# Performance work log

Measured on AMD Instinct MI355X. Metric: run time of the kernel, lower is better.

The kernel has to match this reference:

```python
import jax, jax.numpy as jnp
import numpy as np

EPS = 1e-8

def setup_inputs() -> dict:
    key = jax.random.key(0)
    ks = jax.random.split(key, 10)
    N, IN, Z, C, H = 8192, 512, 128, 64, 50
    x = jax.random.normal(ks[0], (N, IN), dtype=jnp.float32)
    c = jax.random.randint(ks[1], (N, 1), 0, C, dtype=jnp.int64)
    z = jax.random.normal(ks[2], (N, Z), dtype=jnp.float32)
    # f_x MLP params (Linear(IN,50) -> ReLU -> Linear(50,Z))
    W1 = jax.random.normal(ks[3], (IN, H), dtype=jnp.float32) / np.sqrt(IN)
    b1 = jax.random.normal(ks[4], (H,), dtype=jnp.float32) * 0.01
    W2 = jax.random.normal(ks[5], (H, Z), dtype=jnp.float32) / np.sqrt(H)
    b2 = jax.random.normal(ks[6], (Z,), dtype=jnp.float32) * 0.01
    # f_z Linear(Z,Z)
    Wz = jax.random.normal(ks[7], (Z, Z), dtype=jnp.float32) / np.sqrt(Z)
    bz = jax.random.normal(ks[8], (Z,), dtype=jnp.float32) * 0.01
    # per-category bilinear weights w_s [C,Z,Z] (torch.randn init)
    Ws = jax.random.normal(ks[9], (C, Z, Z), dtype=jnp.float32)
    return {"x": x, "c": c, "z": z, "W1": W1, "b1": b1, "W2": W2, "b2": b2, "Wz": Wz, "bz": bz, "Ws": Ws}

def reference(x, c, z, W1, b1, W2, b2, Wz, bz, Ws):
    cf = c.reshape(-1)                                    # [N]
    fx = jax.nn.relu(x @ W1 + b1) @ W2 + b2               # [N,Z]
    fz = z @ Wz + bz                                      # [N,Z]
    # per-sample bilinear: u[n] = fx[n] @ Ws[c[n]]
    u = jnp.einsum('nd,nde->ne', fx, Ws[cf])              # [N,Z]
    T = jax.nn.softplus(jnp.einsum('ne,ne->n', u, fz))    # [N]
    # neg_T[i] = mean over j with c[j]==c[i] of softplus(fx[i] @ Ws[c[i]] @ fz[j])
    S = jax.nn.softplus(u @ fz.T)                         # [N,N]
    mask = (cf[:, None] == cf[None, :]).astype(S.dtype)   # [N,N]
    neg_T = (S * mask).sum(axis=1) / mask.sum(axis=1)     # [N]
    return jnp.log(T + EPS) - jnp.log(neg_T + EPS)
```

## Files before the change

### kernel.cpp

```cpp
#include <hip/hip_runtime.h>
#include <math.h>

#define N_   8192
#define IN_  512
#define ZD   128
#define CC   64
#define HD   50
#define EPSF 1e-8f

typedef float vf4 __attribute__((ext_vector_type(4)));
typedef __attribute__((ext_vector_type(8))) short bfrag;

#define MFMA16(a, b, c) __builtin_amdgcn_mfma_f32_16x16x32_bf16((a), (b), (c), 0, 0, 0)

__device__ __forceinline__ float softplus_hot(float t) {
    return fmaxf(t, 0.f) + __logf(1.f + __expf(-fabsf(t)));
}
__device__ __forceinline__ float softplus_acc(float t) {
    return fmaxf(t, 0.f) + log1pf(expf(-fabsf(t)));
}
__device__ __forceinline__ unsigned short bf16_rn(float x) {
    unsigned int u = __float_as_uint(x);
    return (unsigned short)((u + 0x7fff + ((u >> 16) & 1)) >> 16);
}
__device__ __forceinline__ float bf16_f(unsigned short h) {
    return __uint_as_float(((unsigned int)h) << 16);
}
__device__ __forceinline__ void split8(const float* v, bfrag& hi, bfrag& lo) {
    #pragma unroll
    for (int e = 0; e < 8; ++e) {
        unsigned short h = bf16_rn(v[e]);
        ((short*)&hi)[e] = (short)h;
        ((short*)&lo)[e] = (short)bf16_rn(v[e] - bf16_f(h));
    }
}

__global__ __launch_bounds__(256) void k_pre(const int* __restrict__ c,
                                             const float* __restrict__ W1,
                                             const float* __restrict__ z,
                                             const float* __restrict__ Wz,
                                             const float* __restrict__ bz,
                                             const float* __restrict__ W2,
                                             const float* __restrict__ Ws,
                                             uint4* __restrict__ W1p,
                                             uint4* __restrict__ W2p,
                                             float* __restrict__ fz,
                                             unsigned short* __restrict__ fz_hi,
                                             unsigned short* __restrict__ Wst_hi,
                                             unsigned short* __restrict__ Wst_lo,
                                             int* __restrict__ counts,
                                             int* __restrict__ offsets,
                                             int* __restrict__ grouped) {
    __shared__ float smem[64 * 129];
    int tid = threadIdx.x;
    int b   = blockIdx.x;
    if (b < CC) {
        __shared__ int hist[CC];
        __shared__ int cursor;
        __shared__ int off_s;
        if (tid < CC) hist[tid] = 0;
        if (tid == 0) cursor = 0;
        __syncthreads();
        for (int i = tid; i < N_; i += 256) atomicAdd(&hist[c[i]], 1);
        __syncthreads();
        if (tid == 0) {
            int off = 0;
            for (int q = 0; q < b; ++q) off += hist[q];
            off_s = off;
            counts[b]  = hist[b];
            offsets[b] = off;
        }
        __syncthreads();
        int off = off_s;
        for (int i = tid; i < N_; i += 256) {
            if (c[i] == b) {
                int p = atomicAdd(&cursor, 1);
                grouped[off + p] = i;
            }
        }
    } else if (b < 80) {
        int unit = (b - 64) * 256 + tid;
        int lane = unit & 63, f = (unit >> 6) & 15, kc = unit >> 10;
        int nt = f >> 2, ks = f & 3;
        int n = nt * 16 + (lane & 15);
        int kbase = kc * 128 + ks * 32 + (lane >> 4) * 8;
        unsigned short hi8[8], lo8[8];
        #pragma unroll
        for (int j = 0; j < 8; ++j) {
            int k = kbase + j;
            float v = (n < HD) ? W1[k * HD + n] : 0.f;
            unsigned short h = bf16_rn(v);
            hi8[j] = h;
            lo8[j] = bf16_rn(v - bf16_f(h));
        }
        W1p[kc * 2048 + f * 64 + lane]        = *(uint4*)hi8;
        W1p[kc * 2048 + 1024 + f * 64 + lane] = *(uint4*)lo8;
    } else if (b < 84) {
        int unit = (b - 80) * 256 + tid;
        int lane = unit & 63, f = unit >> 6;
        int nt = f >> 1, ks = f & 1;
        int n = nt * 16 + (lane & 15);
        int kbase = ks * 32 + (lane >> 4) * 8;
        unsigned short hi8[8], lo8[8];
        #pragma unroll
        for (int j = 0; j < 8; ++j) {
            int k = kbase + j;
            float v = (k < HD) ? W2[k * ZD + n] : 0.f;
            unsigned short h = bf16_rn(v);
            hi8[j] = h;
            lo8[j] = bf16_rn(v - bf16_f(h));
        }
        W2p[f * 64 + lane]        = *(uint4*)hi8;
        W2p[1024 + f * 64 + lane] = *(uint4*)lo8;
    } else if (b < 212) {
        float* sz = smem;
        int row0 = (b - 84) * 64;
        vf4* s4 = (vf4*)sz;
        const vf4* z4 = (const vf4*)(z + (size_t)row0 * ZD);
        #pragma unroll
        for (int f = 0; f < 8; ++f) s4[tid + f * 256] = z4[tid + f * 256];
        __syncthreads();
        int cp = tid & 31, rgp = tid >> 5;
        const vf4* Wz4 = (const vf4*)Wz;
        vf4 bb = ((const vf4*)bz)[cp];
        vf4 acc[8];
        #pragma unroll
        for (int r = 0; r < 8; ++r) acc[r] = bb;
        #pragma unroll 1
        for (int d4 = 0; d4 < 32; ++d4) {
            vf4 w0 = Wz4[(4 * d4 + 0) * 32 + cp];
            vf4 w1 = Wz4[(4 * d4 + 1) * 32 + cp];
            vf4 w2 = Wz4[(4 * d4 + 2) * 32 + cp];
            vf4 w3 = Wz4[(4 * d4 + 3) * 32 + cp];
            #pragma unroll
            for (int r = 0; r < 8; ++r) {
                vf4 a = s4[(rgp * 8 + r) * 32 + d4];
                acc[r] += a[0] * w0;
                acc[r] += a[1] * w1;
                acc[r] += a[2] * w2;
                acc[r] += a[3] * w3;
            }
        }
        vf4* fz4 = (vf4*)fz;
        #pragma unroll
        for (int r = 0; r < 8; ++r) {
            int n = row0 + rgp * 8 + r;
            fz4[(size_t)n * 32 + cp] = acc[r];
            ushort4 h;
            h.x = bf16_rn(acc[r][0]); h.y = bf16_rn(acc[r][1]);
            h.z = bf16_rn(acc[r][2]); h.w = bf16_rn(acc[r][3]);
            *(ushort4*)(fz_hi + (size_t)n * ZD + cp * 4) = h;
        }
    } else {
        #pragma unroll 1
        for (int ci = 0; ci < 2; ++ci) {
            int cat = (b - 212) * 2 + ci;
            const float* Wc = Ws + (size_t)cat * ZD * ZD;
            unsigned short* Whi = Wst_hi + (size_t)cat * ZD * ZD;
            unsigned short* Wlo = Wst_lo + (size_t)cat * ZD * ZD;
            #pragma unroll 1
            for (int half = 0; half < 2; ++half) {
                __syncthreads();
                const vf4* src = (const vf4*)(Wc + (size_t)half * 64 * ZD);
                #pragma unroll
                for (int f = 0; f < 8; ++f) {
                    int idx = tid + f * 256;
                    int row = idx >> 5, q = idx & 31;
                    vf4 v = src[idx];
                    #pragma unroll
                    for (int e = 0; e < 4; ++e) smem[row * 129 + q * 4 + e] = v[e];
                }
                __syncthreads();
                #pragma unroll 1
                for (int f = 0; f < 32; ++f) {
                    int idx = tid + f * 256;
                    int e = idx >> 6, dd = idx & 63;
                    float v = smem[dd * 129 + e];
                    unsigned short h = bf16_rn(v);
                    Whi[(size_t)e * ZD + half * 64 + dd] = h;
                    Wlo[(size_t)e * ZD + half * 64 + dd] = bf16_rn(v - bf16_f(h));
                }
            }
        }
    }
}

#define TI 8
__global__ __launch_bounds__(512) void k_all(const float* __restrict__ x,
                                             const uint4* __restrict__ W1p,
                                             const uint4* __restrict__ W2p,
                                             const float* __restrict__ b1,
                                             const float* __restrict__ b2,
                                             const unsigned short* __restrict__ Wst_hi,
                                             const unsigned short* __restrict__ Wst_lo,
                                             const float* __restrict__ fz,
                                             const unsigned short* __restrict__ fz_hi,
                                             const int* __restrict__ grouped,
                                             const int* __restrict__ offsets,
                                             const int* __restrict__ counts,
                                             float* __restrict__ out) {
    __shared__ __align__(16) unsigned char SM[78848];
    uint4* A4    = (uint4*)(SM);
    uint4* B4    = (uint4*)(SM + 34816);
    float* shC   = (float*)(SM + 69632);
    float* sRedF = (float*)(SM + 78336);

    int tid = threadIdx.x;
    int cat = blockIdx.x >> 3;
    int t   = blockIdx.x & (TI - 1);
    int off = offsets[cat], cnt = counts[cat];
    int i0 = t * 32;
    if (i0 >= cnt) return;
    int mI = min(32, cnt - i0);

    int lane = tid & 63, wave = tid >> 6;
    int m = lane & 15, quad = lane >> 4;
    int rg = wave & 1, ch = wave >> 1;

    uint4* sW2 = A4;
    uint4* sW1 = B4;
    float* sh  = shC;

    #pragma unroll
    for (int f = 0; f < 4; ++f) sW2[tid + f * 512] = W2p[tid + f * 512];

    int irowA = rg * 16 + m;
    int n_gA = grouped[off + i0 + min(irowA, mI - 1)];
    const float4* xr = (const float4*)(x + (size_t)n_gA * IN_);

    vf4 accP = {0.f, 0.f, 0.f, 0.f};
    vf4 accQ = {0.f, 0.f, 0.f, 0.f};
    vf4 accR = {0.f, 0.f, 0.f, 0.f};

    #pragma unroll 1
    for (int kc = 0; kc < 4; ++kc) {
        __syncthreads();
        #pragma unroll
        for (int f = 0; f < 4; ++f)
            sW1[tid + f * 512] = W1p[kc * 2048 + tid + f * 512];
        __syncthreads();
        #pragma unroll 1
        for (int ks = 0; ks < 4; ++ks) {
            float4 xa = xr[kc * 32 + ks * 8 + quad * 2];
            float4 xb = xr[kc * 32 + ks * 8 + quad * 2 + 1];
            float xv[8] = {xa.x, xa.y, xa.z, xa.w, xb.x, xb.y, xb.z, xb.w};
            bfrag ah, al;
            split8(xv, ah, al);
            bfrag bh = *(const bfrag*)&sW1[(ch * 4 + ks) * 64 + lane];
            bfrag bl = *(const bfrag*)&sW1[1024 + (ch * 4 + ks) * 64 + lane];
            accP = MFMA16(ah, bh, accP);
            accQ = MFMA16(ah, bl, accQ);
            accR = MFMA16(al, bh, accR);
        }
    }
    {
        int col = ch * 16 + m;
        float bb = (col < HD) ? b1[col] : 0.f;
        vf4 acc = accP + accQ + accR;
        #pragma unroll
        for (int r = 0; r < 4; ++r)
            sh[(rg * 16 + quad * 4 + r) * 68 + col] = fmaxf(acc[r] + bb, 0.f);
    }
    __syncthreads();

    bfrag ah2[2], al2[2];
    #pragma unroll
    for (int ks = 0; ks < 2; ++ks) {
        const float4* shp = (const float4*)&sh[(rg * 16 + m) * 68 + ks * 32 + quad * 8];
        float4 ha = shp[0], hb = shp[1];
        float hv[8] = {ha.x, ha.y, ha.z, ha.w, hb.x, hb.y, hb.z, hb.w};
        split8(hv, ah2[ks], al2[ks]);
    }
    __syncthreads();

    unsigned short* fxhiT = (unsigned short*)shC;
    unsigned short* fxloT = (unsigned short*)B4;
    #pragma unroll
    for (int nt2 = 0; nt2 < 2; ++nt2) {
        int nt = ch * 2 + nt2;
        bfrag bh0 = *(const bfrag*)&sW2[(nt * 2 + 0) * 64 + lane];
        bfrag bl0 = *(const bfrag*)&sW2[1024 + (nt * 2 + 0) * 64 + lane];
        bfrag bh1 = *(const bfrag*)&sW2[(nt * 2 + 1) * 64 + lane];
        bfrag bl1 = *(const bfrag*)&sW2[1024 + (nt * 2 + 1) * 64 + lane];
        vf4 aA = {0.f, 0.f, 0.f, 0.f}, aB = {0.f, 0.f, 0.f, 0.f};
        aA = MFMA16(ah2[0], bh0, aA);
        aA = MFMA16(ah2[0], bl0, aA);
        aA = MFMA16(al2[0], bh0, aA);
        aB = MFMA16(ah2[1], bh1, aB);
        aB = MFMA16(ah2[1], bl1, aB);
        aB = MFMA16(al2[1], bh1, aB);
        vf4 a2 = aA + aB;
        int colB = nt * 16 + m;
        float bb2 = b2[colB];
        #pragma unroll
        for (int r = 0; r < 4; ++r) {
            int row = rg * 16 + quad * 4 + r;
            float v = a2[r] + bb2;
            unsigned short hh = bf16_rn(v);
            fxhiT[row * 136 + colB] = hh;
            fxloT[row * 136 + colB] = bf16_rn(v - bf16_f(hh));
        }
    }
    __syncthreads();

    int eh = ch;
    bfrag a_hi[4], a_lo[4];
    #pragma unroll
    for (int kb = 0; kb < 4; ++kb) {
        a_hi[kb] = *(const bfrag*)&fxhiT[(rg * 16 + m) * 136 + kb * 32 + quad * 8];
        a_lo[kb] = *(const bfrag*)&fxloT[(rg * 16 + m) * 136 + kb * 32 + quad * 8];
    }
    __syncthreads();

    uint4* sWhi = A4;
    uint4* sWlo = B4;
    const uint4* gh = (const uint4*)(Wst_hi + (size_t)cat * ZD * ZD);
    const uint4* gl = (const uint4*)(Wst_lo + (size_t)cat * ZD * ZD);
    #pragma unroll
    for (int f = 0; f < 4; ++f) {
        int idx = tid + f * 512;
        int e = idx >> 4, q = idx & 15;
        sWhi[e * 17 + q] = gh[idx];
        sWlo[e * 17 + q] = gl[idx];
    }
    __syncthreads();

    vf4 uacc[2];
    #pragma unroll 1
    for (int et2 = 0; et2 < 2; ++et2) {
        int et = eh * 2 + et2;
        vf4 aH = {0.f, 0.f, 0.f, 0.f};
        vf4 aM = {0.f, 0.f, 0.f, 0.f};
        vf4 aL = {0.f, 0.f, 0.f, 0.f};
        #pragma unroll
        for (int kb = 0; kb < 4; ++kb) {
            bfrag bh = *(const bfrag*)&sWhi[(et * 16 + m) * 17 + kb * 4 + quad];
            bfrag bl = *(const bfrag*)&sWlo[(et * 16 + m) * 17 + kb * 4 + quad];
            aH = MFMA16(a_hi[kb], bh, aH);
            aM = MFMA16(a_hi[kb], bl, aM);
            aL = MFMA16(a_lo[kb], bh, aL);
        }
        uacc[et2] = aH + aM + aL;
    }

    int nrow[4];
    #pragma unroll
    for (int r = 0; r < 4; ++r) {
        int ir = rg * 16 + quad * 4 + r;
        nrow[r] = (ir < mI) ? grouped[off + i0 + ir] : -1;
    }
    float fzv[2][4];
    #pragma unroll
    for (int et2 = 0; et2 < 2; ++et2) {
        #pragma unroll
        for (int r = 0; r < 4; ++r) {
            fzv[et2][r] = 0.f;
            if (nrow[r] >= 0)
                fzv[et2][r] = fz[(size_t)nrow[r] * ZD + (eh * 2 + et2) * 16 + m];
        }
    }
    float p[4] = {0.f, 0.f, 0.f, 0.f};
    #pragma unroll
    for (int et2 = 0; et2 < 2; ++et2) {
        #pragma unroll
        for (int r = 0; r < 4; ++r) p[r] += uacc[et2][r] * fzv[et2][r];
    }
    #pragma unroll
    for (int r = 0; r < 4; ++r) {
        float v = p[r];
        #pragma unroll
        for (int s = 8; s >= 1; s >>= 1) v += __shfl_xor(v, s, 64);
        p[r] = v;
    }
    if (m == 0) {
        #pragma unroll
        for (int r = 0; r < 4; ++r)
            sRedF[(rg * 4 + eh) * 16 + quad * 4 + r] = p[r];
    }
    __syncthreads();

    unsigned short* su = (unsigned short*)A4;
    #pragma unroll
    for (int et2 = 0; et2 < 2; ++et2) {
        int col = (eh * 2 + et2) * 16 + m;
        #pragma unroll
        for (int r = 0; r < 4; ++r)
            su[(rg * 16 + quad * 4 + r) * 136 + col] = bf16_rn(uacc[et2][r]);
    }
    float logT_r[4] = {0.f, 0.f, 0.f, 0.f};
    if (eh == 0) {
        #pragma unroll
        for (int r = 0; r < 4; ++r) {
            float pt = sRedF[(rg * 4 + 0) * 16 + quad * 4 + r]
                     + sRedF[(rg * 4 + 1) * 16 + quad * 4 + r]
                     + sRedF[(rg * 4 + 2) * 16 + quad * 4 + r]
                     + sRedF[(rg * 4 + 3) * 16 + quad * 4 + r];
            logT_r[r] = logf(softplus_acc(pt) + EPSF);
        }
    }
    __syncthreads();

    bfrag na[4];
    #pragma unroll
    for (int kb = 0; kb < 4; ++kb)
        na[kb] = *(const bfrag*)&su[(rg * 16 + m) * 136 + kb * 32 + quad * 8];

    uint4* sB = B4;
    float negsum[4] = {0.f, 0.f, 0.f, 0.f};

    #pragma unroll 1
    for (int jb = 0; jb < cnt; jb += 64) {
        int mJ = min(64, cnt - jb);
        __syncthreads();
        #pragma unroll
        for (int f = 0; f < 2; ++f) {
            int idx = tid + f * 512;
            int jr = idx >> 4, q = idx & 15;
            uint4 v = {0u, 0u, 0u, 0u};
            if (jr < mJ) {
                int j_g = grouped[off + jb + jr];
                v = *(const uint4*)(fz_hi + (size_t)j_g * ZD + q * 8);
            }
            sB[jr * 17 + q] = v;
        }
        __syncthreads();
        {
            int jt = eh;
            bfrag b0 = *(const bfrag*)&sB[(jt * 16 + m) * 17 + 0 + quad];
            bfrag b1 = *(const bfrag*)&sB[(jt * 16 + m) * 17 + 4 + quad];
            bfrag b2 = *(const bfrag*)&sB[(jt * 16 + m) * 17 + 8 + quad];
            bfrag b3 = *(const bfrag*)&sB[(jt * 16 + m) * 17 + 12 + quad];
            vf4 aA = {0.f, 0.f, 0.f, 0.f}, aB = {0.f, 0.f, 0.f, 0.f};
            aA = MFMA16(na[0], b0, aA);
            aA = MFMA16(na[1], b1, aA);
            aB = MFMA16(na[2], b2, aB);
            aB = MFMA16(na[3], b3, aB);
            vf4 acc = aA + aB;
            bool jok = (jt * 16 + m) < mJ;
            #pragma unroll
            for (int r = 0; r < 4; ++r)
                if (jok) negsum[r] += softplus_hot(acc[r]);
        }
    }

    #pragma unroll
    for (int r = 0; r < 4; ++r) {
        float v = negsum[r];
        #pragma unroll
        for (int s = 8; s >= 1; s >>= 1) v += __shfl_xor(v, s, 64);
        negsum[r] = v;
    }
    if (m == 0) {
        #pragma unroll
        for (int r = 0; r < 4; ++r)
            sRedF[(rg * 4 + eh) * 16 + quad * 4 + r] = negsum[r];
    }
    __syncthreads();
    if (eh == 0 && m == 0) {
        #pragma unroll
        for (int r = 0; r < 4; ++r) {
            if (nrow[r] >= 0) {
                float tot = sRedF[(rg * 4 + 0) * 16 + quad * 4 + r]
                          + sRedF[(rg * 4 + 1) * 16 + quad * 4 + r]
                          + sRedF[(rg * 4 + 2) * 16 + quad * 4 + r]
                          + sRedF[(rg * 4 + 3) * 16 + quad * 4 + r];
                out[nrow[r]] = logT_r[r] - logf(tot / (float)cnt + EPSF);
            }
        }
    }
}

extern "C" void kernel_launch(void* const* d_in, const int* in_sizes, int n_in,
                              void* d_out, int out_size, void* d_ws, size_t ws_size,
                              hipStream_t stream) {
    const float* x  = (const float*)d_in[0];
    const int*   c  = (const int*)  d_in[1];
    const float* z  = (const float*)d_in[2];
    const float* W1 = (const float*)d_in[3];
    const float* b1 = (const float*)d_in[4];
    const float* W2 = (const float*)d_in[5];
    const float* b2 = (const float*)d_in[6];
    const float* Wz = (const float*)d_in[7];
    const float* bz = (const float*)d_in[8];
    const float* Ws = (const float*)d_in[9];
    float* out = (float*)d_out;

    uint4* W1p = (uint4*)d_ws;
    uint4* W2p = W1p + 8192;
    float* fz  = (float*)(W2p + 2048);
    unsigned short* fz_hi  = (unsigned short*)(fz + (size_t)N_ * ZD);
    unsigned short* Wst_hi = fz_hi + (size_t)N_ * ZD;
    unsigned short* Wst_lo = Wst_hi + (size_t)CC * ZD * ZD;
    int* counts  = (int*)(Wst_lo + (size_t)CC * ZD * ZD);
    int* offsets = counts + CC;
    int* grouped = offsets + CC;

    k_pre <<<244, 256, 0, stream>>>(c, W1, z, Wz, bz, W2, Ws, W1p, W2p, fz,
                                    fz_hi, Wst_hi, Wst_lo, counts, offsets,
                                    grouped);
    k_all <<<CC * TI, 512, 0, stream>>>(x, W1p, W2p, b1, b2, Wst_hi, Wst_lo,
                                        fz, fz_hi, grouped, offsets, counts,
                                        out);
}
```

Before: 132.2 us.

## Prefetch global loads into registers and spread Ws conversion over more blocks

Result: slower. 189.0 us (+43.0%).

```diff
diff --git a/kernel.cpp b/kernel.cpp
--- a/kernel.cpp
+++ b/kernel.cpp
@@ -29,7 +29,8 @@
 __device__ __forceinline__ void split8(const float* v, bfrag& hi, bfrag& lo) {
     #pragma unroll
     for (int e = 0; e < 8; ++e) {
-        unsigned short h = bf16_rn(v[e]);
+        unsigned int u = __float_as_uint(v[e]);
+        unsigned short h = (unsigned short)(u >> 16);
         ((short*)&hi)[e] = (short)h;
         ((short*)&lo)[e] = (short)bf16_rn(v[e] - bf16_f(h));
     }
@@ -152,34 +153,31 @@
             *(ushort4*)(fz_hi + (size_t)n * ZD + cp * 4) = h;
         }
     } else {
+        int cat = b - 212;
+        const float* Wc = Ws + (size_t)cat * ZD * ZD;
+        unsigned short* Whi = Wst_hi + (size_t)cat * ZD * ZD;
+        unsigned short* Wlo = Wst_lo + (size_t)cat * ZD * ZD;
         #pragma unroll 1
-        for (int ci = 0; ci < 2; ++ci) {
-            int cat = (b - 212) * 2 + ci;
-            const float* Wc = Ws + (size_t)cat * ZD * ZD;
-            unsigned short* Whi = Wst_hi + (size_t)cat * ZD * ZD;
-            unsigned short* Wlo = Wst_lo + (size_t)cat * ZD * ZD;
+        for (int half = 0; half < 2; ++half) {
+            __syncthreads();
+            const vf4* src = (const vf4*)(Wc + (size_t)half * 64 * ZD);
+            #pragma unroll
+            for (int f = 0; f < 8; ++f) {
+                int idx = tid + f * 256;
+                int row = idx >> 5, q = idx & 31;
+                vf4 v = src[idx];
+                #pragma unroll
+                for (int e = 0; e < 4; ++e) smem[row * 129 + q * 4 + e] = v[e];
+            }
+            __syncthreads();
             #pragma unroll 1
-            for (int half = 0; half < 2; ++half) {
-                __syncthreads();
-                const vf4* src = (const vf4*)(Wc + (size_t)half * 64 * ZD);
-                #pragma unroll
-                for (int f = 0; f < 8; ++f) {
-                    int idx = tid + f * 256;
-                    int row = idx >> 5, q = idx & 31;
-                    vf4 v = src[idx];
-                    #pragma unroll
-                    for (int e = 0; e < 4; ++e) smem[row * 129 + q * 4 + e] = v[e];
-                }
-                __syncthreads();
-                #pragma unroll 1
-                for (int f = 0; f < 32; ++f) {
-                    int idx = tid + f * 256;
-                    int e = idx >> 6, dd = idx & 63;
-                    float v = smem[dd * 129 + e];
-                    unsigned short h = bf16_rn(v);
-                    Whi[(size_t)e * ZD + half * 64 + dd] = h;
-                    Wlo[(size_t)e * ZD + half * 64 + dd] = bf16_rn(v - bf16_f(h));
-                }
+            for (int f = 0; f < 32; ++f) {
+                int idx = tid + f * 256;
+                int e = idx >> 6, dd = idx & 63;
+                float v = smem[dd * 129 + e];
+                unsigned short h = bf16_rn(v);
+                Whi[(size_t)e * ZD + half * 64 + dd] = h;
+                Wlo[(size_t)e * ZD + half * 64 + dd] = bf16_rn(v - bf16_f(h));
             }
         }
     }
@@ -224,6 +222,15 @@
     #pragma unroll
     for (int f = 0; f < 4; ++f) sW2[tid + f * 512] = W2p[tid + f * 512];
 
+    const uint4* gh = (const uint4*)(Wst_hi + (size_t)cat * ZD * ZD);
+    const uint4* gl = (const uint4*)(Wst_lo + (size_t)cat * ZD * ZD);
+    uint4 wh[4], wl[4];
+    #pragma unroll
+    for (int f = 0; f < 4; ++f) {
+        wh[f] = gh[tid + f * 512];
+        wl[f] = gl[tid + f * 512];
+    }
+
     int irowA = rg * 16 + m;
     int n_gA = grouped[off + i0 + min(irowA, mI - 1)];
     const float4* xr = (const float4*)(x + (size_t)n_gA * IN_);
@@ -234,16 +241,23 @@
 
     #pragma unroll 1
     for (int kc = 0; kc < 4; ++kc) {
-        __syncthreads();
-        #pragma unroll
-        for (int f = 0; f < 4; ++f)
-            sW1[tid + f * 512] = W1p[kc * 2048 + tid + f * 512];
+        float4 xa[4], xb[4];
+        #pragma unroll
+        for (int ks = 0; ks < 4; ++ks) {
+            xa[ks] = xr[kc * 32 + ks * 8 + quad * 2];
+            xb[ks] = xr[kc * 32 + ks * 8 + quad * 2 + 1];
+        }
+        uint4 w1r[4];
+        #pragma unroll
+        for (int f = 0; f < 4; ++f) w1r[f] = W1p[kc * 2048 + tid + f * 512];
+        __syncthreads();
+        #pragma unroll
+        for (int f = 0; f < 4; ++f) sW1[tid + f * 512] = w1r[f];
         __syncthreads();
         #pragma unroll 1
         for (int ks = 0; ks < 4; ++ks) {
-            float4 xa = xr[kc * 32 + ks * 8 + quad * 2];
-            float4 xb = xr[kc * 32 + ks * 8 + quad * 2 + 1];
-            float xv[8] = {xa.x, xa.y, xa.z, xa.w, xb.x, xb.y, xb.z, xb.w};
+            float xv[8] = {xa[ks].x, xa[ks].y, xa[ks].z, xa[ks].w,
+                           xb[ks].x, xb[ks].y, xb[ks].z, xb[ks].w};
             bfrag ah, al;
             split8(xv, ah, al);
             bfrag bh = *(const bfrag*)&sW1[(ch * 4 + ks) * 64 + lane];
@@ -296,7 +310,8 @@
         for (int r = 0; r < 4; ++r) {
             int row = rg * 16 + quad * 4 + r;
             float v = a2[r] + bb2;
-            unsigned short hh = bf16_rn(v);
+            unsigned int u = __float_as_uint(v);
+            unsigned short hh = (unsigned short)(u >> 16);
             fxhiT[row * 136 + colB] = hh;
             fxloT[row * 136 + colB] = bf16_rn(v - bf16_f(hh));
         }
@@ -314,14 +329,12 @@
 
     uint4* sWhi = A4;
     uint4* sWlo = B4;
-    const uint4* gh = (const uint4*)(Wst_hi + (size_t)cat * ZD * ZD);
-    const uint4* gl = (const uint4*)(Wst_lo + (size_t)cat * ZD * ZD);
     #pragma unroll
     for (int f = 0; f < 4; ++f) {
         int idx = tid + f * 512;
         int e = idx >> 4, q = idx & 15;
-        sWhi[e * 17 + q] = gh[idx];
-        sWlo[e * 17 + q] = gl[idx];
+        sWhi[e * 17 + q] = wh[f];
+        sWlo[e * 17 + q] = wl[f];
     }
     __syncthreads();
 
@@ -407,21 +420,42 @@
 
     uint4* sB = B4;
     float negsum[4] = {0.f, 0.f, 0.f, 0.f};
+    int jr_s = tid >> 4, q_s = tid & 15;
+
+    uint4 pf[2];
+    {
+        int mJ0 = min(64, cnt);
+        #pragma unroll
+        for (int f = 0; f < 2; ++f) {
+            int jr = jr_s + f * 32;
+            uint4 v = {0u, 0u, 0u, 0u};
+            if (jr < mJ0) {
+                int j_g = grouped[off + jr];
+                v = *(const uint4*)(fz_hi + (size_t)j_g * ZD + q_s * 8);
+            }
+            pf[f] = v;
+        }
+    }
 
     #pragma unroll 1
     for (int jb = 0; jb < cnt; jb += 64) {
         int mJ = min(64, cnt - jb);
         __syncthreads();
         #pragma unroll
-        for (int f = 0; f < 2; ++f) {
-            int idx = tid + f * 512;
-            int jr = idx >> 4, q = idx & 15;
-            uint4 v = {0u, 0u, 0u, 0u};
-            if (jr < mJ) {
-                int j_g = grouped[off + jb + jr];
-                v = *(const uint4*)(fz_hi + (size_t)j_g * ZD + q * 8);
-            }
-            sB[jr * 17 + q] = v;
+        for (int f = 0; f < 2; ++f) sB[(jr_s + f * 32) * 17 + q_s] = pf[f];
+        int jn = jb + 64;
+        if (jn < cnt) {
+            int mJn = min(64, cnt - jn);
+            #pragma unroll
+            for (int f = 0; f < 2; ++f) {
+                int jr = jr_s + f * 32;
+                uint4 v = {0u, 0u, 0u, 0u};
+                if (jr < mJn) {
+                    int j_g = grouped[off + jn + jr];
+                    v = *(const uint4*)(fz_hi + (size_t)j_g * ZD + q_s * 8);
+                }
+                pf[f] = v;
+            }
         }
         __syncthreads();
         {
@@ -495,7 +529,7 @@
     int* offsets = counts + CC;
     int* grouped = offsets + CC;
 
-    k_pre <<<244, 256, 0, stream>>>(c, W1, z, Wz, bz, W2, Ws, W1p, W2p, fz,
+    k_pre <<<276, 256, 0, stream>>>(c, W1, z, Wz, bz, W2, Ws, W1p, W2p, fz,
                                     fz_hi, Wst_hi, Wst_lo, counts, offsets,
                                     grouped);
     k_all <<<CC * TI, 512, 0, stream>>>(x, W1p, W2p, b1, b2, Wst_hi, Wst_lo,
```
